# Kernel tuning notes

Hardware: AMD Instinct MI355X
Metric: run time of the kernel (lower is better)

## Reference

```python
import jax, jax.numpy as jnp
import numpy as np

SEMANTIC_DIM = 128
N_COMPONENTS = 2
EMBED_DIM = SEMANTIC_DIM * N_COMPONENTS  # 256
MAX_LEN = 512


def sinusoidal_pe(max_len, d_model):
    pos = jnp.arange(max_len, dtype=jnp.float32)[:, None]              # (L,1)
    div = jnp.exp(jnp.arange(0, d_model, 2, dtype=jnp.float32) * (-np.log(10000.0) / d_model))
    ang = pos * div                                                     # (L, d/2)
    # interleave sin/cos: pe[:,0::2]=sin, pe[:,1::2]=cos
    return jnp.stack([jnp.sin(ang), jnp.cos(ang)], axis=-1).reshape(max_len, d_model)


def setup_inputs() -> dict:
    key = jax.random.key(0)
    k1, k2, k3, k4 = jax.random.split(key, 4)
    byte_sequence = jax.random.randint(k1, (64, 512), 0, 256, dtype=jnp.int64)
    continuous_positions = jax.random.uniform(k2, (64, 2048), dtype=jnp.float32)
    emb_table = jax.random.normal(k3, (256, EMBED_DIM), dtype=jnp.float32)
    locality_shapes = jax.random.normal(k4, (256, 3), dtype=jnp.float32)
    return {
        "byte_sequence": byte_sequence,
        "continuous_positions": continuous_positions,
        "emb_table": emb_table,
        "locality_shapes": locality_shapes,
    }


def reference(byte_sequence, continuous_positions, emb_table, locality_shapes):
    B, L = byte_sequence.shape
    pe = sinusoidal_pe(MAX_LEN, EMBED_DIM)[:L]                          # (L, E)
    byte_embeds = emb_table[byte_sequence] + pe[None, :, :]             # (B, L, E)
    byte_amplitudes = byte_embeds.reshape(B, L, N_COMPONENTS, SEMANTIC_DIM)

    byte_positions = jnp.linspace(0.0, 1.0, L, dtype=jnp.float32)      # (L,)
    x_diff = continuous_positions[:, :, None] - byte_positions[None, None, :]  # (B, P, L)

    lp = locality_shapes[byte_sequence]                                 # (B, L, 3)
    widths = jnp.abs(lp[:, :, 1]) * 0.02 + 1e-5                         # (B, L)
    amplitudes = jax.nn.sigmoid(lp[:, :, 2])                            # (B, L)

    local_basis = jnp.exp(-0.5 * (x_diff / widths[:, None, :]) ** 2) * amplitudes[:, None, :]
    semantic_field = jnp.einsum('bpl,blcd->bpcd', local_basis, byte_amplitudes)
    return semantic_field
```

## Files before the change

### kernel.cpp

```cpp
#include <hip/hip_runtime.h>
#include <math.h>

#define LSEQ 512
#define EDIM 256
#define PDIM 2048
#define BM   128

typedef _Float16 f16x8 __attribute__((ext_vector_type(8)));
typedef _Float16 f16x4 __attribute__((ext_vector_type(4)));
typedef float    f32x4 __attribute__((ext_vector_type(4)));

__device__ inline void g2lds16(const void* g, void* l) {
    __builtin_amdgcn_global_load_lds(
        (const __attribute__((address_space(1))) void*)g,
        (__attribute__((address_space(3))) void*)l, 16, 0, 0);
}

__global__ void precompute_pe(float* __restrict__ pe) {
    int l = blockIdx.x;
    int j = threadIdx.x;
    float div = expf((2.0f * (float)j) * (-logf(10000.0f) / 256.0f));
    float ang = (float)l * div;
    pe[l * EDIM + 2 * j]     = sinf(ang);
    pe[l * EDIM + 2 * j + 1] = cosf(ang);
}

__global__ void precompute_params(const int* __restrict__ bs,
                                  const float* __restrict__ ls,
                                  float4* __restrict__ params, int n) {
    int i = blockIdx.x * 256 + threadIdx.x;
    if (i >= n) return;
    int byte = bs[i];
    float l1 = ls[byte * 3 + 1];
    float l2 = ls[byte * 3 + 2];
    float wdt = fabsf(l1) * 0.02f + 1e-5f;
    float amp = 1.0f / (1.0f + expf(-l2));
    params[i] = make_float4(1.0f / wdt, amp, 0.0f, 0.0f);
}

__global__ void precompute_baset(const int* __restrict__ bs,
                                 const float* __restrict__ emb,
                                 const float* __restrict__ pe,
                                 _Float16* __restrict__ baset) {
    const int b  = blockIdx.x >> 3;
    const int ks = blockIdx.x & 7;
    const int e  = threadIdx.x;
    const int kbase = ks * 64;
    _Float16* row = baset + ((size_t)(b * 8 + ks) * 256 + e) * 64;
#pragma unroll
    for (int g = 0; g < 8; ++g) {
        f16x8 v;
#pragma unroll
        for (int j = 0; j < 8; ++j) {
            const int l = kbase + g * 8 + j;
            const int byte = bs[b * LSEQ + l];
            v[j] = (_Float16)(emb[byte * EDIM + e] + pe[l * EDIM + e]);
        }
        const int slot = g ^ (e & 7);
        *(f16x8*)&row[slot * 8] = v;
    }
}

__global__ __launch_bounds__(512, 4) void field_mfma(
    const float*    __restrict__ cpos,
    const float4*   __restrict__ params,
    const _Float16* __restrict__ baset,
    float*          __restrict__ out) {

    __shared__ __align__(16) _Float16 sW[BM * 64];
    __shared__ __align__(16) _Float16 sB[256 * 64];
    __shared__ float sPos[BM];

    const int orig = blockIdx.x;
    const int wg   = (orig & 7) * 128 + (orig >> 3);
    const int b    = wg >> 4;
    const int pt   = wg & 15;

    const int tid = threadIdx.x, lane = tid & 63, wave = tid >> 6;
    if (tid < BM) sPos[tid] = cpos[b * PDIM + pt * BM + tid];

    const int kg = tid & 15, pg = tid >> 4;
    const int c15 = lane & 15, g4 = lane >> 4;
    const int wrow = wave >> 2, wcol = wave & 3;

    f32x4 acc[4][4];
#pragma unroll
    for (int i = 0; i < 4; ++i)
#pragma unroll
        for (int j = 0; j < 4; ++j) acc[i][j] = (f32x4)(0.f);

    __syncthreads();
    float mypos[4];
#pragma unroll
    for (int j = 0; j < 4; ++j) mypos[j] = sPos[pg * 4 + j];

    const float invL = 1.0f / (float)(LSEQ - 1);
    const float4* prm = params + b * LSEQ;
    const _Float16* bt = baset + (size_t)b * 8 * 256 * 64;

    for (int ks = 0; ks < 8; ++ks) {
        const _Float16* src = bt + ks * (256 * 64);
#pragma unroll
        for (int is = 0; is < 4; ++is) {
            g2lds16(src + is * 4096 + wave * 512 + lane * 8,
                    sB  + is * 4096 + wave * 512);
        }

        {
            const int k0 = ks * 64 + kg * 4;
            const float4 q0 = prm[k0 + 0];
            const float4 q1 = prm[k0 + 1];
            const float4 q2 = prm[k0 + 2];
            const float4 q3 = prm[k0 + 3];
            const float bl0 = (float)(k0 + 0) * invL;
            const float bl1 = (float)(k0 + 1) * invL;
            const float bl2 = (float)(k0 + 2) * invL;
            const float bl3 = (float)(k0 + 3) * invL;
#pragma unroll
            for (int j = 0; j < 4; ++j) {
                const int p = pg * 4 + j;
                const float pos = mypos[j];
                f16x4 v;
                { float t = (pos - bl0) * q0.x; v[0] = (_Float16)(q0.y * __expf(-0.5f * t * t)); }
                { float t = (pos - bl1) * q1.x; v[1] = (_Float16)(q1.y * __expf(-0.5f * t * t)); }
                { float t = (pos - bl2) * q2.x; v[2] = (_Float16)(q2.y * __expf(-0.5f * t * t)); }
                { float t = (pos - bl3) * q3.x; v[3] = (_Float16)(q3.y * __expf(-0.5f * t * t)); }
                const int off = p * 64 + ((kg >> 1) ^ (p & 7)) * 8 + (kg & 1) * 4;
                *(f16x4*)&sW[off] = v;
            }
        }
        __syncthreads();

#pragma unroll
        for (int kk = 0; kk < 2; ++kk) {
            f16x8 af[4];
#pragma unroll
            for (int rt = 0; rt < 4; ++rt) {
                const int row = wrow * 64 + rt * 16 + c15;
                const int off = row * 64 + (((kk * 4 + g4) ^ (row & 7)) * 8);
                af[rt] = *(const f16x8*)&sW[off];
            }
#pragma unroll
            for (int ct = 0; ct < 4; ++ct) {
                const int erow = wcol * 64 + ct * 16 + c15;
                const int off  = erow * 64 + (((kk * 4 + g4) ^ (erow & 7)) * 8);
                const f16x8 bf = *(const f16x8*)&sB[off];
#pragma unroll
                for (int rt = 0; rt < 4; ++rt)
                    acc[rt][ct] = __builtin_amdgcn_mfma_f32_16x16x32_f16(af[rt], bf, acc[rt][ct], 0, 0, 0);
            }
        }
        __syncthreads();
    }

#pragma unroll
    for (int rt = 0; rt < 4; ++rt)
#pragma unroll
        for (int ct = 0; ct < 4; ++ct) {
            const int e = wcol * 64 + ct * 16 + c15;
#pragma unroll
            for (int r = 0; r < 4; ++r) {
                const int p = pt * BM + wrow * 64 + rt * 16 + g4 * 4 + r;
                out[((size_t)b * PDIM + p) * EDIM + e] = acc[rt][ct][r];
            }
        }
}

extern "C" void kernel_launch(void* const* d_in, const int* in_sizes, int n_in,
                              void* d_out, int out_size, void* d_ws, size_t ws_size,
                              hipStream_t stream) {
    const int*   bs   = (const int*)d_in[0];
    const float* cpos = (const float*)d_in[1];
    const float* emb  = (const float*)d_in[2];
    const float* ls   = (const float*)d_in[3];

    const int B = in_sizes[0] / LSEQ;

    char* ws = (char*)d_ws;
    float*     pe     = (float*)ws;
    float4*    params = (float4*)(ws + (1u << 19));
    _Float16*  baset  = (_Float16*)(ws + (1u << 20));

    precompute_pe<<<LSEQ, EDIM / 2, 0, stream>>>(pe);
    precompute_params<<<(B * LSEQ + 255) / 256, 256, 0, stream>>>(bs, ls, params, B * LSEQ);
    precompute_baset<<<B * 8, 256, 0, stream>>>(bs, emb, pe, baset);

    const int nblocks = B * (PDIM / BM);
    field_mfma<<<nblocks, 512, 0, stream>>>(cpos, params, baset, (float*)d_out);
}
```

Baseline: 75.50 us.

## Double-buffer MFMA K-loop with smaller K tiles and fused precompute kernels

```diff
diff --git a/kernel.cpp b/kernel.cpp
--- a/kernel.cpp
+++ b/kernel.cpp
@@ -5,10 +5,15 @@
 #define EDIM 256
 #define PDIM 2048
 #define BM   128
+#define BK   32
+#define NT   16
 
 typedef _Float16 f16x8 __attribute__((ext_vector_type(8)));
-typedef _Float16 f16x4 __attribute__((ext_vector_type(4)));
 typedef float    f32x4 __attribute__((ext_vector_type(4)));
+
+__device__ __host__ inline int tile_off(int r, int g) {
+    return ((r >> 1) << 6) + ((r & 1) << 5) + (((g ^ ((r >> 1) & 3)) & 3) << 3);
+}
 
 __device__ inline void g2lds16(const void* g, void* l) {
     __builtin_amdgcn_global_load_lds(
@@ -16,60 +21,62 @@
         (__attribute__((address_space(3))) void*)l, 16, 0, 0);
 }
 
-__global__ void precompute_pe(float* __restrict__ pe) {
-    int l = blockIdx.x;
-    int j = threadIdx.x;
-    float div = expf((2.0f * (float)j) * (-logf(10000.0f) / 256.0f));
-    float ang = (float)l * div;
-    pe[l * EDIM + 2 * j]     = sinf(ang);
-    pe[l * EDIM + 2 * j + 1] = cosf(ang);
-}
-
-__global__ void precompute_params(const int* __restrict__ bs,
-                                  const float* __restrict__ ls,
-                                  float4* __restrict__ params, int n) {
-    int i = blockIdx.x * 256 + threadIdx.x;
-    if (i >= n) return;
-    int byte = bs[i];
-    float l1 = ls[byte * 3 + 1];
-    float l2 = ls[byte * 3 + 2];
-    float wdt = fabsf(l1) * 0.02f + 1e-5f;
-    float amp = 1.0f / (1.0f + expf(-l2));
-    params[i] = make_float4(1.0f / wdt, amp, 0.0f, 0.0f);
+__global__ void precompute_tables(const float* __restrict__ ls,
+                                  const int* __restrict__ bs,
+                                  float* __restrict__ pe,
+                                  float2* __restrict__ params, int nparams) {
+    const int bid = blockIdx.x, tid = threadIdx.x;
+    if (bid < LSEQ) {
+        if (tid < 128) {
+            float div = expf((2.0f * (float)tid) * (-logf(10000.0f) / 256.0f));
+            float ang = (float)bid * div;
+            pe[bid * EDIM + 2 * tid]     = sinf(ang);
+            pe[bid * EDIM + 2 * tid + 1] = cosf(ang);
+        }
+    } else {
+        const int i = (bid - LSEQ) * 256 + tid;
+        if (i < nparams) {
+            const int byte = bs[i];
+            const float l1 = ls[byte * 3 + 1];
+            const float l2 = ls[byte * 3 + 2];
+            const float wdt = fabsf(l1) * 0.02f + 1e-5f;
+            params[i] = make_float2(-0.5f / (wdt * wdt),
+                                    1.0f / (1.0f + __expf(-l2)));
+        }
+    }
 }
 
 __global__ void precompute_baset(const int* __restrict__ bs,
                                  const float* __restrict__ emb,
                                  const float* __restrict__ pe,
                                  _Float16* __restrict__ baset) {
-    const int b  = blockIdx.x >> 3;
-    const int ks = blockIdx.x & 7;
-    const int e  = threadIdx.x;
-    const int kbase = ks * 64;
-    _Float16* row = baset + ((size_t)(b * 8 + ks) * 256 + e) * 64;
+    const int b = blockIdx.x >> 4;
+    const int t = blockIdx.x & 15;
+    const int e = threadIdx.x;
+    const int* bsb = bs + b * LSEQ + t * BK;
+    _Float16* chunk = baset + ((size_t)(b * NT + t) << 13);
 #pragma unroll
-    for (int g = 0; g < 8; ++g) {
+    for (int g = 0; g < 4; ++g) {
         f16x8 v;
 #pragma unroll
         for (int j = 0; j < 8; ++j) {
-            const int l = kbase + g * 8 + j;
-            const int byte = bs[b * LSEQ + l];
+            const int l = t * BK + g * 8 + j;
+            const int byte = bsb[g * 8 + j];
             v[j] = (_Float16)(emb[byte * EDIM + e] + pe[l * EDIM + e]);
         }
-        const int slot = g ^ (e & 7);
-        *(f16x8*)&row[slot * 8] = v;
+        *(f16x8*)&chunk[tile_off(e, g)] = v;
     }
 }
 
 __global__ __launch_bounds__(512, 4) void field_mfma(
     const float*    __restrict__ cpos,
-    const float4*   __restrict__ params,
+    const float2*   __restrict__ params,
     const _Float16* __restrict__ baset,
     float*          __restrict__ out) {
 
-    __shared__ __align__(16) _Float16 sW[BM * 64];
-    __shared__ __align__(16) _Float16 sB[256 * 64];
-    __shared__ float sPos[BM];
+    __shared__ __align__(16) _Float16 sW[2][BM * BK];
+    __shared__ __align__(16) _Float16 sB[2][EDIM * BK];
+    __shared__ __align__(16) float2   sPrm[LSEQ];
 
     const int orig = blockIdx.x;
     const int wg   = (orig & 7) * 128 + (orig >> 3);
@@ -77,11 +84,48 @@
     const int pt   = wg & 15;
 
     const int tid = threadIdx.x, lane = tid & 63, wave = tid >> 6;
-    if (tid < BM) sPos[tid] = cpos[b * PDIM + pt * BM + tid];
-
-    const int kg = tid & 15, pg = tid >> 4;
     const int c15 = lane & 15, g4 = lane >> 4;
     const int wrow = wave >> 2, wcol = wave & 3;
+
+    const int sp = tid >> 2;
+    const int sg = tid & 3;
+    const float mypos = cpos[b * PDIM + pt * BM + sp];
+    const float invL  = 1.0f / (float)(LSEQ - 1);
+    const int   woff  = tile_off(sp, sg);
+
+    int aoff[4], boff[4];
+#pragma unroll
+    for (int rt = 0; rt < 4; ++rt) aoff[rt] = tile_off(wrow * 64 + rt * 16 + c15, g4);
+#pragma unroll
+    for (int ct = 0; ct < 4; ++ct) boff[ct] = tile_off(wcol * 64 + ct * 16 + c15, g4);
+
+    sPrm[tid] = params[b * LSEQ + tid];
+    const _Float16* bt = baset + ((size_t)b * NT << 13);
+#pragma unroll
+    for (int buf = 0; buf < 2; ++buf) {
+        const _Float16* src = bt + buf * 8192 + wave * 1024 + lane * 8;
+        g2lds16(src,       &sB[buf][wave * 1024]);
+        g2lds16(src + 512, &sB[buf][wave * 1024 + 512]);
+    }
+    __syncthreads();
+
+    auto genW = [&](int t, int dbuf) {
+        const float4* qp = (const float4*)&sPrm[t * BK + sg * 8];
+        const float4 q01 = qp[0], q23 = qp[1], q45 = qp[2], q67 = qp[3];
+        const float bl0 = (float)(t * BK + sg * 8) * invL;
+        f16x8 wv;
+#define GENW(i, c2, am) { float d = mypos - (bl0 + (float)(i) * invL); \
+                          wv[i] = (_Float16)((am) * __expf(d * d * (c2))); }
+        GENW(0, q01.x, q01.y) GENW(1, q01.z, q01.w)
+        GENW(2, q23.x, q23.y) GENW(3, q23.z, q23.w)
+        GENW(4, q45.x, q45.y) GENW(5, q45.z, q45.w)
+        GENW(6, q67.x, q67.y) GENW(7, q67.z, q67.w)
+#undef GENW
+        *(f16x8*)&sW[dbuf][woff] = wv;
+    };
+
+    genW(0, 0);
+    __syncthreads();
 
     f32x4 acc[4][4];
 #pragma unroll
@@ -89,68 +133,32 @@
 #pragma unroll
         for (int j = 0; j < 4; ++j) acc[i][j] = (f32x4)(0.f);
 
-    __syncthreads();
-    float mypos[4];
+    for (int t = 0; t < NT; ++t) {
+        const int cur = t & 1;
+        if (t < NT - 1) genW(t + 1, cur ^ 1);
+
+        const _Float16* wb = sW[cur];
+        const _Float16* bb = sB[cur];
+        f16x8 af[4];
 #pragma unroll
-    for (int j = 0; j < 4; ++j) mypos[j] = sPos[pg * 4 + j];
+        for (int rt = 0; rt < 4; ++rt) af[rt] = *(const f16x8*)&wb[aoff[rt]];
+        __builtin_amdgcn_s_setprio(1);
+#pragma unroll
+        for (int ct = 0; ct < 4; ++ct) {
+            const f16x8 bf = *(const f16x8*)&bb[boff[ct]];
+#pragma unroll
+            for (int rt = 0; rt < 4; ++rt)
+                acc[rt][ct] = __builtin_amdgcn_mfma_f32_16x16x32_f16(af[rt], bf, acc[rt][ct], 0, 0, 0);
+        }
+        __builtin_amdgcn_s_setprio(0);
 
-    const float invL = 1.0f / (float)(LSEQ - 1);
-    const float4* prm = params + b * LSEQ;
-    const _Float16* bt = baset + (size_t)b * 8 * 256 * 64;
-
-    for (int ks = 0; ks < 8; ++ks) {
-        const _Float16* src = bt + ks * (256 * 64);
-#pragma unroll
-        for (int is = 0; is < 4; ++is) {
-            g2lds16(src + is * 4096 + wave * 512 + lane * 8,
-                    sB  + is * 4096 + wave * 512);
-        }
-
-        {
-            const int k0 = ks * 64 + kg * 4;
-            const float4 q0 = prm[k0 + 0];
-            const float4 q1 = prm[k0 + 1];
-            const float4 q2 = prm[k0 + 2];
-            const float4 q3 = prm[k0 + 3];
-            const float bl0 = (float)(k0 + 0) * invL;
-            const float bl1 = (float)(k0 + 1) * invL;
-            const float bl2 = (float)(k0 + 2) * invL;
-            const float bl3 = (float)(k0 + 3) * invL;
-#pragma unroll
-            for (int j = 0; j < 4; ++j) {
-                const int p = pg * 4 + j;
-                const float pos = mypos[j];
-                f16x4 v;
-                { float t = (pos - bl0) * q0.x; v[0] = (_Float16)(q0.y * __expf(-0.5f * t * t)); }
-                { float t = (pos - bl1) * q1.x; v[1] = (_Float16)(q1.y * __expf(-0.5f * t * t)); }
-                { float t = (pos - bl2) * q2.x; v[2] = (_Float16)(q2.y * __expf(-0.5f * t * t)); }
-                { float t = (pos - bl3) * q3.x; v[3] = (_Float16)(q3.y * __expf(-0.5f * t * t)); }
-                const int off = p * 64 + ((kg >> 1) ^ (p & 7)) * 8 + (kg & 1) * 4;
-                *(f16x4*)&sW[off] = v;
-            }
-        }
         __syncthreads();
 
-#pragma unroll
-        for (int kk = 0; kk < 2; ++kk) {
-            f16x8 af[4];
-#pragma unroll
-            for (int rt = 0; rt < 4; ++rt) {
-                const int row = wrow * 64 + rt * 16 + c15;
-                const int off = row * 64 + (((kk * 4 + g4) ^ (row & 7)) * 8);
-                af[rt] = *(const f16x8*)&sW[off];
-            }
-#pragma unroll
-            for (int ct = 0; ct < 4; ++ct) {
-                const int erow = wcol * 64 + ct * 16 + c15;
-                const int off  = erow * 64 + (((kk * 4 + g4) ^ (erow & 7)) * 8);
-                const f16x8 bf = *(const f16x8*)&sB[off];
-#pragma unroll
-                for (int rt = 0; rt < 4; ++rt)
-                    acc[rt][ct] = __builtin_amdgcn_mfma_f32_16x16x32_f16(af[rt], bf, acc[rt][ct], 0, 0, 0);
-            }
+        if (t < NT - 2) {
+            const _Float16* src = bt + (t + 2) * 8192 + wave * 1024 + lane * 8;
+            g2lds16(src,       &sB[cur][wave * 1024]);
+            g2lds16(src + 512, &sB[cur][wave * 1024 + 512]);
         }
-        __syncthreads();
     }
 
 #pragma unroll
@@ -177,14 +185,12 @@
     const int B = in_sizes[0] / LSEQ;
 
     char* ws = (char*)d_ws;
-    float*     pe     = (float*)ws;
-    float4*    params = (float4*)(ws + (1u << 19));
-    _Float16*  baset  = (_Float16*)(ws + (1u << 20));
+    float*    pe     = (float*)ws;
+    float2*   params = (float2*)(ws + (1u << 19));
+    _Float16* baset  = (_Float16*)(ws + (1u << 20));
 
-    precompute_pe<<<LSEQ, EDIM / 2, 0, stream>>>(pe);
-    precompute_params<<<(B * LSEQ + 255) / 256, 256, 0, stream>>>(bs, ls, params, B * LSEQ);
-    precompute_baset<<<B * 8, 256, 0, stream>>>(bs, emb, pe, baset);
-
-    const int nblocks = B * (PDIM / BM);
-    field_mfma<<<nblocks, 512, 0, stream>>>(cpos, params, baset, (float*)d_out);
+    const int nparams = B * LSEQ;
+    precompute_tables<<<LSEQ + (nparams + 255) / 256, 256, 0, stream>>>(ls, bs, pe, params, nparams);
+    precompute_baset<<<B * NT, 256, 0, stream>>>(bs, emb, pe, baset);
+    field_mfma<<<B * (PDIM / BM), 512, 0, stream>>>(cpos, params, baset, (float*)d_out);
 }
```

New measurement: 73.96 us. -2.0%, faster.
